# Optimization experiments

Hardware: AMD Instinct MI355X
Metric: run time of the kernel (lower is better)

Reference implementation:

```python
import jax, jax.numpy as jnp
import numpy as np

B, N, D, NS, H, ITERS = 16, 2048, 128, 8, 128, 3
EPS = 1e-8


def _ln(x, g, b):
    m = jnp.mean(x, -1, keepdims=True)
    v = jnp.mean((x - m) ** 2, -1, keepdims=True)
    return (x - m) * jax.lax.rsqrt(v + 1e-5) * g + b


def _gru(x, h, Wih, Whh, bih, bhh):
    # PyTorch GRUCell math
    gi = x @ Wih.T + bih
    gh = h @ Whh.T + bhh
    ir, iz, inn = jnp.split(gi, 3, -1)
    hr, hz, hn = jnp.split(gh, 3, -1)
    r = jax.nn.sigmoid(ir + hr)
    z = jax.nn.sigmoid(iz + hz)
    n = jnp.tanh(inn + r * hn)
    return (1.0 - z) * n + z * h


def setup_inputs() -> dict:
    key = jax.random.key(0)
    ks = jax.random.split(key, 16)

    def lin(k, out_d, in_d):
        lim = 1.0 / np.sqrt(in_d)
        return jax.random.uniform(k, (out_d, in_d), jnp.float32, -lim, lim)

    return {
        "inputs": jax.random.normal(ks[0], (B, N, D), jnp.float32),
        "init_noise": jax.random.normal(ks[1], (B, NS, 2 * D), jnp.float32),
        "slots_mu": jax.random.normal(ks[2], (1, 1, 2 * D), jnp.float32),
        "slots_logsigma": jax.random.normal(ks[3], (1, 1, 2 * D), jnp.float32) * 0.08,  # ~xavier scale
        "Wq": lin(ks[4], D, D),
        "Wk": lin(ks[5], D, D),
        "gru_Wih": lin(ks[6], 3 * D, D),
        "gru_Whh": lin(ks[7], 3 * D, D),
        "gru_bih": jnp.zeros((3 * D,), jnp.float32),
        "gru_bhh": jnp.zeros((3 * D,), jnp.float32),
        "mlp_mu_W1": lin(ks[8], H, D),
        "mlp_mu_b1": jnp.zeros((H,), jnp.float32),
        "mlp_mu_W2": lin(ks[9], D, H),
        "mlp_mu_b2": jnp.zeros((D,), jnp.float32),
        "ln_in_g": jnp.ones((D,), jnp.float32),
        "ln_in_b": jnp.zeros((D,), jnp.float32),
        "ln_slots_g": jnp.ones((2 * D,), jnp.float32),
        "ln_slots_b": jnp.zeros((2 * D,), jnp.float32),
        "ln_mu_g": jnp.ones((D,), jnp.float32),
        "ln_mu_b": jnp.zeros((D,), jnp.float32),
        "mlp_out_W1": lin(ks[10], 2 * H, 2 * D),
        "mlp_out_b1": jnp.zeros((2 * H,), jnp.float32),
        "mlp_out_W2": lin(ks[11], D, 2 * H),
        "mlp_out_b2": jnp.zeros((D,), jnp.float32),
    }


def _forward(inputs, init_noise, slots_mu, slots_logsigma, Wq, Wk,
             gru_Wih, gru_Whh, gru_bih, gru_bhh,
             mlp_mu_W1, mlp_mu_b1, mlp_mu_W2, mlp_mu_b2,
             ln_in_g, ln_in_b, ln_slots_g, ln_slots_b, ln_mu_g, ln_mu_b,
             mlp_out_W1, mlp_out_b1, mlp_out_W2, mlp_out_b2):
    x = _ln(inputs, ln_in_g, ln_in_b)                      # (B,N,D)
    k = x @ Wk.T
    v = k                                                  # original uses to_k for both k and v
    slots = slots_mu + jnp.exp(slots_logsigma) * init_noise  # (B,NS,2D)
    pi_cl = jnp.full((B, NS, 1), 1.0 / NS, inputs.dtype)

    def step(slots, pi_cl):
        s = _ln(slots, ln_slots_g, ln_slots_b)
        mu_s, ls_s = jnp.split(s, 2, -1)                   # (B,NS,D) each
        q_mu = mu_s @ Wq.T
        q_ls = ls_s @ Wq.T
        inv_var = jnp.exp(-2.0 * q_ls)                     # 1 / exp(q_logsigma)^2
        diff = k[:, None, :, :] - q_mu[:, :, None, :]      # (B,NS,N,D)
        dots = jnp.einsum('bind,bid->bin', diff * diff, inv_var)
        dots_exp = (jnp.exp(-dots) + EPS) * pi_cl          # (B,NS,N)
        gammas = dots_exp / dots_exp.sum(1, keepdims=True)
        attn = gammas / gammas.sum(-1, keepdims=True)
        upd = jnp.einsum('bjd,bij->bid', v, attn)          # (B,NS,D)
        upd = _gru(upd.reshape(-1, D), mu_s.reshape(-1, D),
                   gru_Wih, gru_Whh, gru_bih, gru_bhh).reshape(B, NS, D)
        h = _ln(upd, ln_mu_g, ln_mu_b)
        upd = upd + (jax.nn.relu(h @ mlp_mu_W1.T + mlp_mu_b1) @ mlp_mu_W2.T + mlp_mu_b2)
        diff2 = v[:, None, :, :] - upd[:, :, None, :]      # (B,NS,N,D)
        upd_ls = 0.5 * jnp.log(jnp.einsum('bind,bin->bid', diff2 * diff2 + EPS, attn))
        slots_new = jnp.concatenate([upd, upd_ls], -1)
        pi_new = gammas.sum(-1, keepdims=True)
        pi_new = pi_new / pi_new.shape[2]                  # shape[2]==1: faithful no-op from original
        return slots_new, pi_new

    for _ in range(ITERS):
        slots, pi_cl = step(slots, pi_cl)
    slots, pi_cl = step(jax.lax.stop_gradient(slots), pi_cl)
    h = jax.nn.relu(slots @ mlp_out_W1.T + mlp_out_b1)
    return h @ mlp_out_W2.T + mlp_out_b2                   # (B,NS,D)


def reference(inputs, init_noise, slots_mu, slots_logsigma, Wq, Wk,
              gru_Wih, gru_Whh, gru_bih, gru_bhh,
              mlp_mu_W1, mlp_mu_b1, mlp_mu_W2, mlp_mu_b2,
              ln_in_g, ln_in_b, ln_slots_g, ln_slots_b, ln_mu_g, ln_mu_b,
              mlp_out_W1, mlp_out_b1, mlp_out_W2, mlp_out_b2):
    return _forward(inputs, init_noise, slots_mu, slots_logsigma, Wq, Wk,
                    gru_Wih, gru_Whh, gru_bih, gru_bhh,
                    mlp_mu_W1, mlp_mu_b1, mlp_mu_W2, mlp_mu_b2,
                    ln_in_g, ln_in_b, ln_slots_g, ln_slots_b, ln_mu_g, ln_mu_b,
                    mlp_out_W1, mlp_out_b1, mlp_out_W2, mlp_out_b2)
```

## Files before the change

### kernel.cpp

```cpp
#include <hip/hip_runtime.h>

#define EPS_ 1e-8f

constexpr int OFF_K     = 0;
constexpr int OFF_WQT   = 4194304;
constexpr int OFF_WKT   = OFF_WQT  + 16384;
constexpr int OFF_WIHT  = OFF_WKT  + 16384;
constexpr int OFF_WHHT  = OFF_WIHT + 49152;
constexpr int OFF_WM1T  = OFF_WHHT + 49152;
constexpr int OFF_WM2T  = OFF_WM1T + 16384;
constexpr int OFF_WO1T  = OFF_WM2T + 16384;
constexpr int OFF_WO2T  = OFF_WO1T + 65536;
constexpr int OFF_SLOTS = OFF_WO2T + 32768;
constexpr int OFF_PI    = OFF_SLOTS+ 32768;
constexpr int OFF_MUS   = OFF_PI   + 128;
constexpr int OFF_WA    = OFF_MUS  + 16384;
constexpr int OFF_WB    = OFF_WA   + 16384;
constexpr int OFF_UN    = OFF_WB   + 16384;
constexpr int OFF_S2    = OFF_UN   + 524288;
constexpr int OFF_DEN   = OFF_S2   + 524288;
constexpr int OFF_CZ    = OFF_DEN  + 4096;

__global__ __launch_bounds__(256) void init_kernel(
    const float* __restrict__ Wq,  const float* __restrict__ Wk,
    const float* __restrict__ Wih, const float* __restrict__ Whh,
    const float* __restrict__ Wm1, const float* __restrict__ Wm2,
    const float* __restrict__ Wo1, const float* __restrict__ Wo2,
    const float* __restrict__ smu, const float* __restrict__ sls,
    const float* __restrict__ noise, float* __restrict__ ws) {
  int idx = blockIdx.x * 256 + threadIdx.x;
  if (idx < 16384) { int j = idx >> 7, d = idx & 127; ws[OFF_WQT + d*128 + j] = Wq[idx]; return; }
  idx -= 16384;
  if (idx < 16384) { int j = idx >> 7, d = idx & 127; ws[OFF_WKT + d*128 + j] = Wk[idx]; return; }
  idx -= 16384;
  if (idx < 49152) { int j = idx >> 7, d = idx & 127; ws[OFF_WIHT + d*384 + j] = Wih[idx]; return; }
  idx -= 49152;
  if (idx < 49152) { int j = idx >> 7, d = idx & 127; ws[OFF_WHHT + d*384 + j] = Whh[idx]; return; }
  idx -= 49152;
  if (idx < 16384) { int j = idx >> 7, d = idx & 127; ws[OFF_WM1T + d*128 + j] = Wm1[idx]; return; }
  idx -= 16384;
  if (idx < 16384) { int j = idx >> 7, d = idx & 127; ws[OFF_WM2T + d*128 + j] = Wm2[idx]; return; }
  idx -= 16384;
  if (idx < 65536) { int j = idx >> 8, d = idx & 255; ws[OFF_WO1T + d*256 + j] = Wo1[idx]; return; }
  idx -= 65536;
  if (idx < 32768) { int j = idx >> 8, m = idx & 255; ws[OFF_WO2T + m*128 + j] = Wo2[idx]; return; }
  idx -= 32768;
  if (idx < 32768) { int c = idx & 255; ws[OFF_SLOTS + idx] = smu[c] + expf(sls[c]) * noise[idx]; return; }
  idx -= 32768;
  if (idx < 128) { ws[OFF_PI + idx] = 0.125f; }
}

__global__ __launch_bounds__(256) void ks1_kernel(
    const float* __restrict__ xin, const float* __restrict__ g, const float* __restrict__ bb,
    const float* __restrict__ WkT, float* __restrict__ kout,
    const float* __restrict__ slots, const float* __restrict__ gsl, const float* __restrict__ bsl,
    const float* __restrict__ WqT, float* __restrict__ mus,
    float* __restrict__ wA, float* __restrict__ wB, float* __restrict__ cz) {
  __shared__ float xsT[128][72];
  __shared__ float2 red2[64][4];
  __shared__ float mrow[64], srow[64];
  int t = threadIdx.x;
  if (blockIdx.x < 512) {
    long long base = (long long)blockIdx.x * 64 * 128;
    int r = t >> 2, q = t & 3;
    float vals[32];
    {
      const float4* src = (const float4*)(xin + base + r * 128 + q * 32);
      #pragma unroll
      for (int i = 0; i < 8; ++i) *(float4*)&vals[i * 4] = src[i];
    }
    {
      float s = 0.f, ss = 0.f;
      #pragma unroll
      for (int i = 0; i < 32; ++i) { float v = vals[i]; s += v; ss = fmaf(v, v, ss); }
      red2[r][q] = make_float2(s, ss);
    }
    __syncthreads();
    if (t < 64) {
      float s = 0.f, ss = 0.f;
      #pragma unroll
      for (int c = 0; c < 4; ++c) { float2 p = red2[t][c]; s += p.x; ss += p.y; }
      float m = s * (1.0f / 128.0f);
      float var = ss * (1.0f / 128.0f) - m * m;
      mrow[t] = m; srow[t] = rsqrtf(var + 1e-5f);
    }
    __syncthreads();
    {
      float m = mrow[r], is = srow[r];
      #pragma unroll 8
      for (int u = 0; u < 32; ++u) {
        int d = q * 32 + u;
        xsT[d][r] = (vals[u] - m) * is * g[d] + bb[d];
      }
    }
    __syncthreads();
    int j4 = t & 31, rg = t >> 5;
    int r0 = rg * 8;
    float a0[8], a1[8], a2[8], a3[8];
    #pragma unroll
    for (int i = 0; i < 8; ++i) { a0[i] = 0.f; a1[i] = 0.f; a2[i] = 0.f; a3[i] = 0.f; }
    #pragma unroll 2
    for (int d = 0; d < 128; ++d) {
      float4 wv = *(const float4*)(WkT + d * 128 + j4 * 4);
      float4 x0 = *(const float4*)&xsT[d][r0];
      float4 x1 = *(const float4*)&xsT[d][r0 + 4];
      a0[0] = fmaf(x0.x, wv.x, a0[0]); a1[0] = fmaf(x0.x, wv.y, a1[0]);
      a2[0] = fmaf(x0.x, wv.z, a2[0]); a3[0] = fmaf(x0.x, wv.w, a3[0]);
      a0[1] = fmaf(x0.y, wv.x, a0[1]); a1[1] = fmaf(x0.y, wv.y, a1[1]);
      a2[1] = fmaf(x0.y, wv.z, a2[1]); a3[1] = fmaf(x0.y, wv.w, a3[1]);
      a0[2] = fmaf(x0.z, wv.x, a0[2]); a1[2] = fmaf(x0.z, wv.y, a1[2]);
      a2[2] = fmaf(x0.z, wv.z, a2[2]); a3[2] = fmaf(x0.z, wv.w, a3[2]);
      a0[3] = fmaf(x0.w, wv.x, a0[3]); a1[3] = fmaf(x0.w, wv.y, a1[3]);
      a2[3] = fmaf(x0.w, wv.z, a2[3]); a3[3] = fmaf(x0.w, wv.w, a3[3]);
      a0[4] = fmaf(x1.x, wv.x, a0[4]); a1[4] = fmaf(x1.x, wv.y, a1[4]);
      a2[4] = fmaf(x1.x, wv.z, a2[4]); a3[4] = fmaf(x1.x, wv.w, a3[4]);
      a0[5] = fmaf(x1.y, wv.x, a0[5]); a1[5] = fmaf(x1.y, wv.y, a1[5]);
      a2[5] = fmaf(x1.y, wv.z, a2[5]); a3[5] = fmaf(x1.y, wv.w, a3[5]);
      a0[6] = fmaf(x1.z, wv.x, a0[6]); a1[6] = fmaf(x1.z, wv.y, a1[6]);
      a2[6] = fmaf(x1.z, wv.z, a2[6]); a3[6] = fmaf(x1.z, wv.w, a3[6]);
      a0[7] = fmaf(x1.w, wv.x, a0[7]); a1[7] = fmaf(x1.w, wv.y, a1[7]);
      a2[7] = fmaf(x1.w, wv.z, a2[7]); a3[7] = fmaf(x1.w, wv.w, a3[7]);
    }
    #pragma unroll
    for (int i = 0; i < 8; ++i) {
      float* o = kout + base + (long long)(r0 + i) * 128 + j4 * 4;
      *(float4*)o = make_float4(a0[i], a1[i], a2[i], a3[i]);
    }
  } else {
    int bi = blockIdx.x - 512;
    float* f = &xsT[0][0];
    float* sl    = f;
    float* qs_l  = f + 256;
    float* ivs_l = f + 384;
    float2* wr   = (float2*)(f + 512);
    float* wrC   = f + 520;
    float v = slots[bi * 256 + t];
    float s = v, ss = v * v;
    #pragma unroll
    for (int o = 32; o > 0; o >>= 1) { s += __shfl_down(s, o); ss += __shfl_down(ss, o); }
    if ((t & 63) == 0) wr[t >> 6] = make_float2(s, ss);
    __syncthreads();
    float fs  = wr[0].x + wr[1].x + wr[2].x + wr[3].x;
    float fss = wr[0].y + wr[1].y + wr[2].y + wr[3].y;
    float m   = fs * (1.0f/256.0f);
    float var = fss * (1.0f/256.0f) - m * m;
    float isr = rsqrtf(var + 1e-5f);
    float sn  = (v - m) * isr * gsl[t] + bsl[t];
    sl[t] = sn;
    __syncthreads();
    if (t < 128) {
      float acc = 0.f;
      #pragma unroll 4
      for (int d = 0; d < 128; ++d) acc = fmaf(sl[d], WqT[d * 128 + t], acc);
      qs_l[t] = acc;
      mus[bi * 128 + t] = sn;
    } else {
      int jj = t - 128;
      float acc = 0.f;
      #pragma unroll 4
      for (int d = 0; d < 128; ++d) acc = fmaf(sl[128 + d], WqT[d * 128 + jj], acc);
      ivs_l[jj] = expf(-2.0f * acc);
    }
    __syncthreads();
    float cp = 0.f;
    if (t < 128) {
      float iv = ivs_l[t], q = qs_l[t];
      wA[bi * 128 + t] = iv;
      wB[bi * 128 + t] = -2.0f * q * iv;
      cp = q * q * iv;
    }
    #pragma unroll
    for (int o = 32; o > 0; o >>= 1) cp += __shfl_down(cp, o);
    if ((t & 63) == 0) wrC[t >> 6] = cp;
    __syncthreads();
    if (t == 0) cz[bi] = wrC[0] + wrC[1];
  }
}

__global__ __launch_bounds__(1024) void s2_kernel(
    const float* __restrict__ kmat, const float* __restrict__ wA,
    const float* __restrict__ wB,  const float* __restrict__ cz,
    const float* __restrict__ pi,
    float* __restrict__ wun, float* __restrict__ ws2, float* __restrict__ wden) {
  __shared__ float pdots[16][64][8];
  __shared__ float es[64][9];
  __shared__ float recip[64];
  __shared__ float gT[8][72];
  __shared__ float pd[8][8];
  __shared__ float pisl[8], czl[8];
  int t = threadIdx.x;
  int chunk = blockIdx.x, b = blockIdx.y;
  if (t < 8) { pisl[t] = pi[b * 8 + t]; czl[t] = cz[b * 8 + t]; }
  if (t < 512) {
    int w = t & 15, nt = t >> 4;
    int n0 = nt * 2;
    const float4* kr4 = (const float4*)(kmat + (long long)(b * 2048 + chunk * 64) * 128);
    const float4* wa4 = (const float4*)(wA + b * 1024);
    const float4* wb4 = (const float4*)(wB + b * 1024);
    float acc0[8] = {0,0,0,0,0,0,0,0};
    float acc1[8] = {0,0,0,0,0,0,0,0};
    #pragma unroll
    for (int i = 0; i < 2; ++i) {
      int gg = i * 16 + w;
      float4 k0 = kr4[n0 * 32 + gg];
      float4 k1 = kr4[(n0 + 1) * 32 + gg];
      float x0 = k0.x * k0.x, y0 = k0.y * k0.y, z0 = k0.z * k0.z, w0 = k0.w * k0.w;
      float x1 = k1.x * k1.x, y1 = k1.y * k1.y, z1 = k1.z * k1.z, w1 = k1.w * k1.w;
      #pragma unroll
      for (int s = 0; s < 8; ++s) {
        float4 a4 = wa4[s * 32 + gg];
        float4 b4 = wb4[s * 32 + gg];
        float c0 = acc0[s], c1 = acc1[s];
        c0 = fmaf(x0, a4.x, c0); c0 = fmaf(k0.x, b4.x, c0);
        c0 = fmaf(y0, a4.y, c0); c0 = fmaf(k0.y, b4.y, c0);
        c0 = fmaf(z0, a4.z, c0); c0 = fmaf(k0.z, b4.z, c0);
        c0 = fmaf(w0, a4.w, c0); c0 = fmaf(k0.w, b4.w, c0);
        c1 = fmaf(x1, a4.x, c1); c1 = fmaf(k1.x, b4.x, c1);
        c1 = fmaf(y1, a4.y, c1); c1 = fmaf(k1.y, b4.y, c1);
        c1 = fmaf(z1, a4.z, c1); c1 = fmaf(k1.z, b4.z, c1);
        c1 = fmaf(w1, a4.w, c1); c1 = fmaf(k1.w, b4.w, c1);
        acc0[s] = c0; acc1[s] = c1;
      }
    }
    *(float4*)&pdots[w][n0][0]     = make_float4(acc0[0], acc0[1], acc0[2], acc0[3]);
    *(float4*)&pdots[w][n0][4]     = make_float4(acc0[4], acc0[5], acc0[6], acc0[7]);
    *(float4*)&pdots[w][n0 + 1][0] = make_float4(acc1[0], acc1[1], acc1[2], acc1[3]);
    *(float4*)&pdots[w][n0 + 1][4] = make_float4(acc1[4], acc1[5], acc1[6], acc1[7]);
  }
  __syncthreads();
  float e = 0.f;
  if (t < 512) {
    int n2 = t >> 3, s = t & 7;
    float dots = czl[s];
    #pragma unroll
    for (int w = 0; w < 16; ++w) dots += pdots[w][n2][s];
    e = (expf(-dots) + EPS_) * pisl[s];
    es[n2][s] = e;
  }
  __syncthreads();
  if (t < 64) {
    float ssum = 0.f;
    #pragma unroll
    for (int s = 0; s < 8; ++s) ssum += es[t][s];
    recip[t] = 1.0f / ssum;
  }
  __syncthreads();
  if (t < 512) {
    int n2 = t >> 3, s = t & 7;
    float gam = e * recip[n2];
    gT[s][n2] = gam;
    float p = gam;
    p += __shfl_down(p, 8); p += __shfl_down(p, 16); p += __shfl_down(p, 32);
    if ((t & 63) < 8) pd[t >> 6][t & 7] = p;
  }
  __syncthreads();
  if (t < 8) {
    float sden = 0.f;
    #pragma unroll
    for (int w = 0; w < 8; ++w) sden += pd[w][t];
    wden[(b * 32 + chunk) * 8 + t] = sden;
  }
  {
    int d = t & 127, sh = t >> 7;
    const float* kcol = kmat + (long long)(b * 2048 + chunk * 64) * 128 + d;
    float u0 = 0.f, q0 = 0.f, u1 = 0.f, q1 = 0.f;
    #pragma unroll 2
    for (int n3 = 0; n3 < 64; n3 += 4) {
      float4 ga = *(const float4*)&gT[sh][n3];
      float k0 = kcol[(n3 + 0) * 128];
      float k1 = kcol[(n3 + 1) * 128];
      float k2 = kcol[(n3 + 2) * 128];
      float k3 = kcol[(n3 + 3) * 128];
      u0 = fmaf(ga.x, k0, u0); q0 = fmaf(ga.x, k0 * k0, q0);
      u1 = fmaf(ga.y, k1, u1); q1 = fmaf(ga.y, k1 * k1, q1);
      u0 = fmaf(ga.z, k2, u0); q0 = fmaf(ga.z, k2 * k2, q0);
      u1 = fmaf(ga.w, k3, u1); q1 = fmaf(ga.w, k3 * k3, q1);
    }
    int pb = ((b * 32 + chunk) * 8 + sh) * 128 + d;
    wun[pb] = u0 + u1;
    ws2[pb] = q0 + q1;
  }
}

__global__ __launch_bounds__(512) void s3_kernel(
    const float* __restrict__ wun, const float* __restrict__ ws2, const float* __restrict__ wden,
    const float* __restrict__ WihT, const float* __restrict__ WhhT,
    const float* __restrict__ bih,  const float* __restrict__ bhh,
    const float* __restrict__ Wm1T, const float* __restrict__ bm1,
    const float* __restrict__ Wm2T, const float* __restrict__ bm2,
    const float* __restrict__ gmu,  const float* __restrict__ bmu,
    float* __restrict__ slots, float* __restrict__ pi,
    int do_s1,
    const float* __restrict__ gs, const float* __restrict__ bs,
    const float* __restrict__ WqT,
    float* __restrict__ mus, float* __restrict__ wAo, float* __restrict__ wBo,
    float* __restrict__ czo,
    const float* __restrict__ Wo1T, const float* __restrict__ bo1,
    const float* __restrict__ Wo2T, const float* __restrict__ bo2,
    float* __restrict__ out) {
  int t = threadIdx.x, bi = blockIdx.x;
  int d = t & 127, q = t >> 7;
  int b = bi >> 3, i = bi & 7;
  __shared__ float redU[4][128], redS[4][128];
  __shared__ float dred[32];
  __shared__ float xs[128], hs[128];
  __shared__ float gacc[4][6][128];
  __shared__ float ga[6][128];
  __shared__ float grus[128], hl[128], m1s[128];
  __shared__ float macc[4][128];
  __shared__ float2 wr2[2];
  __shared__ float uarr[256];
  float unp = 0.f, s2p = 0.f;
  #pragma unroll
  for (int c = q * 8; c < q * 8 + 8; ++c) {
    int po = ((b * 32 + c) * 8 + i) * 128 + d;
    unp += wun[po]; s2p += ws2[po];
  }
  redU[q][d] = unp; redS[q][d] = s2p;
  if (t < 32) dred[t] = wden[(b * 32 + t) * 8 + i];
  if (q == 1) hs[d] = mus[bi * 128 + d];
  __syncthreads();
  float den = 0.f;
  #pragma unroll
  for (int c = 0; c < 32; ++c) den += dred[c];
  float un  = redU[0][d] + redU[1][d] + redU[2][d] + redU[3][d];
  float s2v = redS[0][d] + redS[1][d] + redS[2][d] + redS[3][d];
  if (q == 0) xs[d] = un / den;
  __syncthreads();
  {
    float a0 = 0, a1 = 0, a2 = 0, a3 = 0, a4 = 0, a5 = 0;
    #pragma unroll 4
    for (int dd = q * 32; dd < q * 32 + 32; ++dd) {
      float xv = xs[dd], hv = hs[dd];
      const float* wi = &WihT[dd * 384 + d];
      const float* wh = &WhhT[dd * 384 + d];
      a0 = fmaf(xv, wi[0],   a0);
      a1 = fmaf(xv, wi[128], a1);
      a2 = fmaf(xv, wi[256], a2);
      a3 = fmaf(hv, wh[0],   a3);
      a4 = fmaf(hv, wh[128], a4);
      a5 = fmaf(hv, wh[256], a5);
    }
    gacc[q][0][d] = a0; gacc[q][1][d] = a1; gacc[q][2][d] = a2;
    gacc[q][3][d] = a3; gacc[q][4][d] = a4; gacc[q][5][d] = a5;
  }
  __syncthreads();
  for (int f = t; f < 768; f += 512) {
    int j = f >> 7, dd = f & 127;
    ga[j][dd] = gacc[0][j][dd] + gacc[1][j][dd] + gacc[2][j][dd] + gacc[3][j][dd];
  }
  __syncthreads();
  float gru = 0.f;
  if (q == 0) {
    float ir = ga[0][d] + bih[d], iz = ga[1][d] + bih[128 + d], inn = ga[2][d] + bih[256 + d];
    float hr = ga[3][d] + bhh[d], hz = ga[4][d] + bhh[128 + d], hn  = ga[5][d] + bhh[256 + d];
    float r  = 1.0f / (1.0f + expf(-(ir + hr)));
    float z  = 1.0f / (1.0f + expf(-(iz + hz)));
    float nn = tanhf(inn + r * hn);
    gru = (1.0f - z) * nn + z * hs[d];
    grus[d] = gru;
    float s = gru, ssq = gru * gru;
    #pragma unroll
    for (int o = 32; o > 0; o >>= 1) { s += __shfl_down(s, o); ssq += __shfl_down(ssq, o); }
    if ((d & 63) == 0) wr2[d >> 6] = make_float2(s, ssq);
  }
  __syncthreads();
  if (q == 0) {
    float fs = wr2[0].x + wr2[1].x, fss = wr2[0].y + wr2[1].y;
    float mean = fs * (1.0f/128.0f);
    float var  = fss * (1.0f/128.0f) - mean * mean;
    hl[d] = (gru - mean) * rsqrtf(var + 1e-5f) * gmu[d] + bmu[d];
  }
  __syncthreads();
  {
    float m1p = 0.f;
    #pragma unroll 4
    for (int dd = q * 32; dd < q * 32 + 32; ++dd)
      m1p = fmaf(hl[dd], Wm1T[dd * 128 + d], m1p);
    macc[q][d] = m1p;
  }
  __syncthreads();
  if (q == 0) m1s[d] = fmaxf(macc[0][d] + macc[1][d] + macc[2][d] + macc[3][d] + bm1[d], 0.f);
  __syncthreads();
  {
    float m2p = 0.f;
    #pragma unroll 4
    for (int dd = q * 32; dd < q * 32 + 32; ++dd)
      m2p = fmaf(m1s[dd], Wm2T[dd * 128 + d], m2p);
    macc[q][d] = m2p;
  }
  __syncthreads();
  if (q == 0) {
    float u = grus[d] + macc[0][d] + macc[1][d] + macc[2][d] + macc[3][d] + bm2[d];
    float val = (s2v - 2.0f * u * un + u * u * den) / den;
    float ls = 0.5f * logf(fmaxf(val, 0.0f) + EPS_);
    slots[bi * 256 + d]       = u;
    slots[bi * 256 + 128 + d] = ls;
    uarr[d] = u; uarr[128 + d] = ls;
    if (d == 0) pi[bi] = den;
  }
  __syncthreads();
  if (do_s1) {
    __shared__ float2 wr4[4];
    __shared__ float sln[256];
    __shared__ float qacc[2][2][128];
    __shared__ float qs_l[128], ivs_l[128];
    __shared__ float wrC[8];
    if (t < 256) {
      float v2 = uarr[t];
      float s = v2, ssq = v2 * v2;
      #pragma unroll
      for (int o = 32; o > 0; o >>= 1) { s += __shfl_down(s, o); ssq += __shfl_down(ssq, o); }
      if ((t & 63) == 0) wr4[t >> 6] = make_float2(s, ssq);
    }
    __syncthreads();
    if (t < 256) {
      float fs  = wr4[0].x + wr4[1].x + wr4[2].x + wr4[3].x;
      float fss = wr4[0].y + wr4[1].y + wr4[2].y + wr4[3].y;
      float m   = fs * (1.0f/256.0f);
      float var = fss * (1.0f/256.0f) - m * m;
      sln[t] = (uarr[t] - m) * rsqrtf(var + 1e-5f) * gs[t] + bs[t];
    }
    __syncthreads();
    {
      int h2 = t >> 8, qq = (t >> 7) & 1, d2 = t & 127;
      const float* src = sln + h2 * 128;
      float acc = 0.f;
      #pragma unroll 4
      for (int dd = qq * 64; dd < qq * 64 + 64; ++dd)
        acc = fmaf(src[dd], WqT[dd * 128 + d2], acc);
      qacc[h2][qq][d2] = acc;
    }
    __syncthreads();
    if (t < 128) {
      qs_l[t] = qacc[0][0][t] + qacc[0][1][t];
      mus[bi * 128 + t] = sln[t];
    } else if (t < 256) {
      int dd2 = t - 128;
      ivs_l[dd2] = expf(-2.0f * (qacc[1][0][dd2] + qacc[1][1][dd2]));
    }
    __syncthreads();
    float cp = 0.f;
    if (t < 128) {
      float iv = ivs_l[t], qv = qs_l[t];
      wAo[bi * 128 + t] = iv;
      wBo[bi * 128 + t] = -2.0f * qv * iv;
      cp = qv * qv * iv;
    }
    #pragma unroll
    for (int o = 32; o > 0; o >>= 1) cp += __shfl_down(cp, o);
    if ((t & 63) == 0) wrC[t >> 6] = cp;
    __syncthreads();
    if (t == 0) czo[bi] = wrC[0] + wrC[1];
  } else {
    __shared__ float oacc[2][256];
    __shared__ float hh[256];
    {
      int o = t & 255, qq = t >> 8;
      float acc = 0.f;
      #pragma unroll 4
      for (int dd = qq * 128; dd < qq * 128 + 128; ++dd)
        acc = fmaf(uarr[dd], Wo1T[dd * 256 + o], acc);
      oacc[qq][o] = acc;
    }
    __syncthreads();
    if (t < 256) hh[t] = fmaxf(oacc[0][t] + oacc[1][t] + bo1[t], 0.f);
    __syncthreads();
    {
      int o2 = t & 127, q4 = t >> 7;
      float acc2 = 0.f;
      #pragma unroll 4
      for (int dd = q4 * 64; dd < q4 * 64 + 64; ++dd)
        acc2 = fmaf(hh[dd], Wo2T[dd * 128 + o2], acc2);
      macc[q4][o2] = acc2;
    }
    __syncthreads();
    if (t < 128) out[bi * 128 + t] = macc[0][t] + macc[1][t] + macc[2][t] + macc[3][t] + bo2[t];
  }
}

extern "C" void kernel_launch(void* const* d_in, const int* in_sizes, int n_in,
                              void* d_out, int out_size, void* d_ws, size_t ws_size,
                              hipStream_t stream) {
  const float* inputs = (const float*)d_in[0];
  const float* noise  = (const float*)d_in[1];
  const float* smu    = (const float*)d_in[2];
  const float* sls    = (const float*)d_in[3];
  const float* Wq     = (const float*)d_in[4];
  const float* Wk     = (const float*)d_in[5];
  const float* Wih    = (const float*)d_in[6];
  const float* Whh    = (const float*)d_in[7];
  const float* bih    = (const float*)d_in[8];
  const float* bhh    = (const float*)d_in[9];
  const float* Wm1    = (const float*)d_in[10];
  const float* bm1    = (const float*)d_in[11];
  const float* Wm2    = (const float*)d_in[12];
  const float* bm2    = (const float*)d_in[13];
  const float* gin    = (const float*)d_in[14];
  const float* bin    = (const float*)d_in[15];
  const float* gsl    = (const float*)d_in[16];
  const float* bsl    = (const float*)d_in[17];
  const float* gmu    = (const float*)d_in[18];
  const float* bmu    = (const float*)d_in[19];
  const float* Wo1    = (const float*)d_in[20];
  const float* bo1    = (const float*)d_in[21];
  const float* Wo2    = (const float*)d_in[22];
  const float* bo2    = (const float*)d_in[23];

  float* ws    = (float*)d_ws;
  float* kbuf  = ws + OFF_K;
  float* WqT   = ws + OFF_WQT;
  float* WkT   = ws + OFF_WKT;
  float* WihT  = ws + OFF_WIHT;
  float* WhhT  = ws + OFF_WHHT;
  float* Wm1T  = ws + OFF_WM1T;
  float* Wm2T  = ws + OFF_WM2T;
  float* Wo1T  = ws + OFF_WO1T;
  float* Wo2T  = ws + OFF_WO2T;
  float* slots = ws + OFF_SLOTS;
  float* pibuf = ws + OFF_PI;
  float* mus   = ws + OFF_MUS;
  float* wA    = ws + OFF_WA;
  float* wB    = ws + OFF_WB;
  float* wun   = ws + OFF_UN;
  float* ws2   = ws + OFF_S2;
  float* wden  = ws + OFF_DEN;
  float* czb   = ws + OFF_CZ;

  hipLaunchKernelGGL(init_kernel, dim3(1153), dim3(256), 0, stream,
                     Wq, Wk, Wih, Whh, Wm1, Wm2, Wo1, Wo2, smu, sls, noise, ws);
  hipLaunchKernelGGL(ks1_kernel, dim3(640), dim3(256), 0, stream,
                     inputs, gin, bin, WkT, kbuf,
                     slots, gsl, bsl, WqT, mus, wA, wB, czb);
  for (int s = 0; s < 4; ++s) {
    hipLaunchKernelGGL(s2_kernel, dim3(32, 16), dim3(1024), 0, stream,
                       kbuf, wA, wB, czb, pibuf, wun, ws2, wden);
    hipLaunchKernelGGL(s3_kernel, dim3(128), dim3(512), 0, stream,
                       wun, ws2, wden, WihT, WhhT, bih, bhh,
                       Wm1T, bm1, Wm2T, bm2, gmu, bmu, slots, pibuf,
                       (s < 3) ? 1 : 0, gsl, bsl, WqT, mus, wA, wB, czb,
                       Wo1T, bo1, Wo2T, bo2, (float*)d_out);
  }
}
```

Measured before the change: 174.9 us.

## Fuse s2 and s3 into one step kernel using a last-block atomic counter

Merges the per-chunk responsibility/statistics kernel and the per-slot GRU/MLP update kernel into a single launch per iteration. The last block to finish for each batch, detected with an atomic counter and threadfence, performs the slot update for all 8 slots. This removes four kernel launches and their inter-kernel gaps. The update stage now runs on only 16 blocks with serial 128-long reductions instead of 128 blocks, so that tail work may lengthen. The u/s2 accumulation is also rewritten to read k with coalesced float4 loads and reduce partials in shared memory.

```diff
diff --git a/kernel.cpp b/kernel.cpp
--- a/kernel.cpp
+++ b/kernel.cpp
@@ -20,6 +20,15 @@
 constexpr int OFF_S2    = OFF_UN   + 524288;
 constexpr int OFF_DEN   = OFF_S2   + 524288;
 constexpr int OFF_CZ    = OFF_DEN  + 4096;
+constexpr int OFF_CNT   = OFF_CZ   + 128;
+
+struct Args {
+  const float *xin, *noise, *smu, *sls, *Wq, *Wk, *Wih, *Whh, *bih, *bhh,
+              *Wm1, *bm1, *Wm2, *bm2, *gin, *bin, *gsl, *bsl, *gmu, *bmu,
+              *Wo1, *bo1, *Wo2, *bo2;
+  float* ws;
+  float* out;
+};
 
 __global__ __launch_bounds__(256) void init_kernel(
     const float* __restrict__ Wq,  const float* __restrict__ Wk,
@@ -47,7 +56,9 @@
   idx -= 32768;
   if (idx < 32768) { int c = idx & 255; ws[OFF_SLOTS + idx] = smu[c] + expf(sls[c]) * noise[idx]; return; }
   idx -= 32768;
-  if (idx < 128) { ws[OFF_PI + idx] = 0.125f; }
+  if (idx < 128) { ws[OFF_PI + idx] = 0.125f; return; }
+  idx -= 128;
+  if (idx < 64) { ((int*)(ws + OFF_CNT))[idx] = 0; }
 }
 
 __global__ __launch_bounds__(256) void ks1_kernel(
@@ -177,20 +188,44 @@
   }
 }
 
-__global__ __launch_bounds__(1024) void s2_kernel(
-    const float* __restrict__ kmat, const float* __restrict__ wA,
-    const float* __restrict__ wB,  const float* __restrict__ cz,
-    const float* __restrict__ pi,
-    float* __restrict__ wun, float* __restrict__ ws2, float* __restrict__ wden) {
-  __shared__ float pdots[16][64][8];
+struct ScrS3 {
+  float xs[8][128];
+  float hs[8][128];
+  float gh[2][8][128];
+  float m1s[8][128];
+  float uarr[8][256];
+  float2 wr2[8][2];
+  float wrC[8][2];
+};
+union UScr {
+  struct { float pdots[16][64][8]; } p1;
+  struct { float pP[2][4][8][128]; } p2;
+  ScrS3 s3;
+};
+
+__global__ __launch_bounds__(1024) void step_kernel(Args a, int step) {
+  float* ws = a.ws;
+  const float* kmat = ws + OFF_K;
+  float* wA  = ws + OFF_WA;  float* wB  = ws + OFF_WB;
+  float* czp = ws + OFF_CZ;  float* pip = ws + OFF_PI;
+  float* wun = ws + OFF_UN;  float* ws2 = ws + OFF_S2;
+  float* wden= ws + OFF_DEN; float* mus = ws + OFF_MUS;
+  const float* WihT = ws + OFF_WIHT; const float* WhhT = ws + OFF_WHHT;
+  const float* Wm1T = ws + OFF_WM1T; const float* Wm2T = ws + OFF_WM2T;
+  const float* WqT  = ws + OFF_WQT;
+  const float* Wo1T = ws + OFF_WO1T; const float* Wo2T = ws + OFF_WO2T;
+  float* slots = ws + OFF_SLOTS;
+
+  __shared__ UScr u;
   __shared__ float es[64][9];
   __shared__ float recip[64];
   __shared__ float gT[8][72];
   __shared__ float pd[8][8];
   __shared__ float pisl[8], czl[8];
+  __shared__ int sflag;
   int t = threadIdx.x;
   int chunk = blockIdx.x, b = blockIdx.y;
-  if (t < 8) { pisl[t] = pi[b * 8 + t]; czl[t] = cz[b * 8 + t]; }
+  if (t < 8) { pisl[t] = pip[b * 8 + t]; czl[t] = czp[b * 8 + t]; }
   if (t < 512) {
     int w = t & 15, nt = t >> 4;
     int n0 = nt * 2;
@@ -222,10 +257,10 @@
         acc0[s] = c0; acc1[s] = c1;
       }
     }
-    *(float4*)&pdots[w][n0][0]     = make_float4(acc0[0], acc0[1], acc0[2], acc0[3]);
-    *(float4*)&pdots[w][n0][4]     = make_float4(acc0[4], acc0[5], acc0[6], acc0[7]);
-    *(float4*)&pdots[w][n0 + 1][0] = make_float4(acc1[0], acc1[1], acc1[2], acc1[3]);
-    *(float4*)&pdots[w][n0 + 1][4] = make_float4(acc1[4], acc1[5], acc1[6], acc1[7]);
+    *(float4*)&u.p1.pdots[w][n0][0]     = make_float4(acc0[0], acc0[1], acc0[2], acc0[3]);
+    *(float4*)&u.p1.pdots[w][n0][4]     = make_float4(acc0[4], acc0[5], acc0[6], acc0[7]);
+    *(float4*)&u.p1.pdots[w][n0 + 1][0] = make_float4(acc1[0], acc1[1], acc1[2], acc1[3]);
+    *(float4*)&u.p1.pdots[w][n0 + 1][4] = make_float4(acc1[4], acc1[5], acc1[6], acc1[7]);
   }
   __syncthreads();
   float e = 0.f;
@@ -233,7 +268,7 @@
     int n2 = t >> 3, s = t & 7;
     float dots = czl[s];
     #pragma unroll
-    for (int w = 0; w < 16; ++w) dots += pdots[w][n2][s];
+    for (int w = 0; w < 16; ++w) dots += u.p1.pdots[w][n2][s];
     e = (expf(-dots) + EPS_) * pisl[s];
     es[n2][s] = e;
   }
@@ -261,284 +296,198 @@
     wden[(b * 32 + chunk) * 8 + t] = sden;
   }
   {
-    int d = t & 127, sh = t >> 7;
-    const float* kcol = kmat + (long long)(b * 2048 + chunk * 64) * 128 + d;
-    float u0 = 0.f, q0 = 0.f, u1 = 0.f, q1 = 0.f;
+    int g = t & 31, sl = (t >> 5) & 7, nh = t >> 8;
+    const float4* kr4 = (const float4*)(kmat + (long long)(b * 2048 + chunk * 64) * 128);
+    float4 ua = {0, 0, 0, 0}, qa = {0, 0, 0, 0};
     #pragma unroll 2
-    for (int n3 = 0; n3 < 64; n3 += 4) {
-      float4 ga = *(const float4*)&gT[sh][n3];
-      float k0 = kcol[(n3 + 0) * 128];
-      float k1 = kcol[(n3 + 1) * 128];
-      float k2 = kcol[(n3 + 2) * 128];
-      float k3 = kcol[(n3 + 3) * 128];
-      u0 = fmaf(ga.x, k0, u0); q0 = fmaf(ga.x, k0 * k0, q0);
-      u1 = fmaf(ga.y, k1, u1); q1 = fmaf(ga.y, k1 * k1, q1);
-      u0 = fmaf(ga.z, k2, u0); q0 = fmaf(ga.z, k2 * k2, q0);
-      u1 = fmaf(ga.w, k3, u1); q1 = fmaf(ga.w, k3 * k3, q1);
-    }
-    int pb = ((b * 32 + chunk) * 8 + sh) * 128 + d;
-    wun[pb] = u0 + u1;
-    ws2[pb] = q0 + q1;
-  }
-}
-
-__global__ __launch_bounds__(512) void s3_kernel(
-    const float* __restrict__ wun, const float* __restrict__ ws2, const float* __restrict__ wden,
-    const float* __restrict__ WihT, const float* __restrict__ WhhT,
-    const float* __restrict__ bih,  const float* __restrict__ bhh,
-    const float* __restrict__ Wm1T, const float* __restrict__ bm1,
-    const float* __restrict__ Wm2T, const float* __restrict__ bm2,
-    const float* __restrict__ gmu,  const float* __restrict__ bmu,
-    float* __restrict__ slots, float* __restrict__ pi,
-    int do_s1,
-    const float* __restrict__ gs, const float* __restrict__ bs,
-    const float* __restrict__ WqT,
-    float* __restrict__ mus, float* __restrict__ wAo, float* __restrict__ wBo,
-    float* __restrict__ czo,
-    const float* __restrict__ Wo1T, const float* __restrict__ bo1,
-    const float* __restrict__ Wo2T, const float* __restrict__ bo2,
-    float* __restrict__ out) {
-  int t = threadIdx.x, bi = blockIdx.x;
-  int d = t & 127, q = t >> 7;
-  int b = bi >> 3, i = bi & 7;
-  __shared__ float redU[4][128], redS[4][128];
-  __shared__ float dred[32];
-  __shared__ float xs[128], hs[128];
-  __shared__ float gacc[4][6][128];
-  __shared__ float ga[6][128];
-  __shared__ float grus[128], hl[128], m1s[128];
-  __shared__ float macc[4][128];
-  __shared__ float2 wr2[2];
-  __shared__ float uarr[256];
-  float unp = 0.f, s2p = 0.f;
-  #pragma unroll
-  for (int c = q * 8; c < q * 8 + 8; ++c) {
-    int po = ((b * 32 + c) * 8 + i) * 128 + d;
-    unp += wun[po]; s2p += ws2[po];
-  }
-  redU[q][d] = unp; redS[q][d] = s2p;
-  if (t < 32) dred[t] = wden[(b * 32 + t) * 8 + i];
-  if (q == 1) hs[d] = mus[bi * 128 + d];
-  __syncthreads();
-  float den = 0.f;
-  #pragma unroll
-  for (int c = 0; c < 32; ++c) den += dred[c];
-  float un  = redU[0][d] + redU[1][d] + redU[2][d] + redU[3][d];
-  float s2v = redS[0][d] + redS[1][d] + redS[2][d] + redS[3][d];
-  if (q == 0) xs[d] = un / den;
-  __syncthreads();
-  {
-    float a0 = 0, a1 = 0, a2 = 0, a3 = 0, a4 = 0, a5 = 0;
+    for (int n = nh * 16; n < nh * 16 + 16; ++n) {
+      float4 kv = kr4[n * 32 + g];
+      float gam = gT[sl][n];
+      ua.x = fmaf(gam, kv.x, ua.x); qa.x = fmaf(gam, kv.x * kv.x, qa.x);
+      ua.y = fmaf(gam, kv.y, ua.y); qa.y = fmaf(gam, kv.y * kv.y, qa.y);
+      ua.z = fmaf(gam, kv.z, ua.z); qa.z = fmaf(gam, kv.z * kv.z, qa.z);
+      ua.w = fmaf(gam, kv.w, ua.w); qa.w = fmaf(gam, kv.w * kv.w, qa.w);
+    }
+    *(float4*)&u.p2.pP[0][nh][sl][g * 4] = ua;
+    *(float4*)&u.p2.pP[1][nh][sl][g * 4] = qa;
+  }
+  __syncthreads();
+  {
+    int uq = t >> 9, rem = t & 511;
+    int sl = rem >> 6, d0 = (rem & 63) * 2;
+    float* dst = (uq == 0 ? wun : ws2);
+    long long pbase = (long long)((b * 32 + chunk) * 8 + sl) * 128;
+    #pragma unroll
+    for (int eo = 0; eo < 2; ++eo) {
+      int d = d0 + eo;
+      dst[pbase + d] = u.p2.pP[uq][0][sl][d] + u.p2.pP[uq][1][sl][d] +
+                       u.p2.pP[uq][2][sl][d] + u.p2.pP[uq][3][sl][d];
+    }
+  }
+  __syncthreads();
+  if (t == 0) {
+    __threadfence();
+    sflag = atomicAdd((int*)(ws + OFF_CNT) + step * 16 + b, 1);
+  }
+  __syncthreads();
+  if (sflag != 31) return;
+  __threadfence();
+  ScrS3* p = &u.s3;
+  int i = t >> 7, d = t & 127, bi = b * 8 + i;
+  float un = 0.f, s2v = 0.f, den = 0.f;
+  for (int c = 0; c < 32; ++c) {
+    long long po = (long long)((b * 32 + c) * 8 + i) * 128 + d;
+    un += wun[po]; s2v += ws2[po];
+  }
+  for (int c = 0; c < 32; ++c) den += wden[(b * 32 + c) * 8 + i];
+  p->xs[i][d] = un / den;
+  p->hs[i][d] = mus[bi * 128 + d];
+  __syncthreads();
+  float a0 = 0, a1 = 0, a2 = 0, a3 = 0, a4 = 0, a5 = 0;
+  #pragma unroll 2
+  for (int dd = 0; dd < 128; ++dd) {
+    float xv = p->xs[i][dd], hv = p->hs[i][dd];
+    const float* wi = &WihT[dd * 384 + d];
+    const float* wh = &WhhT[dd * 384 + d];
+    a0 = fmaf(xv, wi[0],   a0);
+    a1 = fmaf(xv, wi[128], a1);
+    a2 = fmaf(xv, wi[256], a2);
+    a3 = fmaf(hv, wh[0],   a3);
+    a4 = fmaf(hv, wh[128], a4);
+    a5 = fmaf(hv, wh[256], a5);
+  }
+  float ir = a0 + a.bih[d], iz = a1 + a.bih[128 + d], inn = a2 + a.bih[256 + d];
+  float hr = a3 + a.bhh[d], hz = a4 + a.bhh[128 + d], hn  = a5 + a.bhh[256 + d];
+  float rg = 1.0f / (1.0f + expf(-(ir + hr)));
+  float zg = 1.0f / (1.0f + expf(-(iz + hz)));
+  float nn = tanhf(inn + rg * hn);
+  float gru = (1.0f - zg) * nn + zg * p->hs[i][d];
+  p->gh[0][i][d] = gru;
+  {
+    float s = gru, ssq = gru * gru;
+    #pragma unroll
+    for (int o = 32; o > 0; o >>= 1) { s += __shfl_down(s, o); ssq += __shfl_down(ssq, o); }
+    if ((d & 63) == 0) p->wr2[i][d >> 6] = make_float2(s, ssq);
+  }
+  __syncthreads();
+  {
+    float fs = p->wr2[i][0].x + p->wr2[i][1].x;
+    float fss = p->wr2[i][0].y + p->wr2[i][1].y;
+    float mean = fs * (1.0f / 128.0f);
+    float var  = fss * (1.0f / 128.0f) - mean * mean;
+    p->gh[1][i][d] = (gru - mean) * rsqrtf(var + 1e-5f) * a.gmu[d] + a.bmu[d];
+  }
+  __syncthreads();
+  {
+    float m1 = 0.f;
     #pragma unroll 4
-    for (int dd = q * 32; dd < q * 32 + 32; ++dd) {
-      float xv = xs[dd], hv = hs[dd];
-      const float* wi = &WihT[dd * 384 + d];
-      const float* wh = &WhhT[dd * 384 + d];
-      a0 = fmaf(xv, wi[0],   a0);
-      a1 = fmaf(xv, wi[128], a1);
-      a2 = fmaf(xv, wi[256], a2);
-      a3 = fmaf(hv, wh[0],   a3);
-      a4 = fmaf(hv, wh[128], a4);
-      a5 = fmaf(hv, wh[256], a5);
-    }
-    gacc[q][0][d] = a0; gacc[q][1][d] = a1; gacc[q][2][d] = a2;
-    gacc[q][3][d] = a3; gacc[q][4][d] = a4; gacc[q][5][d] = a5;
-  }
-  __syncthreads();
-  for (int f = t; f < 768; f += 512) {
-    int j = f >> 7, dd = f & 127;
-    ga[j][dd] = gacc[0][j][dd] + gacc[1][j][dd] + gacc[2][j][dd] + gacc[3][j][dd];
-  }
-  __syncthreads();
-  float gru = 0.f;
-  if (q == 0) {
-    float ir = ga[0][d] + bih[d], iz = ga[1][d] + bih[128 + d], inn = ga[2][d] + bih[256 + d];
-    float hr = ga[3][d] + bhh[d], hz = ga[4][d] + bhh[128 + d], hn  = ga[5][d] + bhh[256 + d];
-    float r  = 1.0f / (1.0f + expf(-(ir + hr)));
-    float z  = 1.0f / (1.0f + expf(-(iz + hz)));
-    float nn = tanhf(inn + r * hn);
-    gru = (1.0f - z) * nn + z * hs[d];
-    grus[d] = gru;
-    float s = gru, ssq = gru * gru;
-    #pragma unroll
-    for (int o = 32; o > 0; o >>= 1) { s += __shfl_down(s, o); ssq += __shfl_down(ssq, o); }
-    if ((d & 63) == 0) wr2[d >> 6] = make_float2(s, ssq);
-  }
-  __syncthreads();
-  if (q == 0) {
-    float fs = wr2[0].x + wr2[1].x, fss = wr2[0].y + wr2[1].y;
-    float mean = fs * (1.0f/128.0f);
-    float var  = fss * (1.0f/128.0f) - mean * mean;
-    hl[d] = (gru - mean) * rsqrtf(var + 1e-5f) * gmu[d] + bmu[d];
-  }
-  __syncthreads();
-  {
-    float m1p = 0.f;
+    for (int dd = 0; dd < 128; ++dd)
+      m1 = fmaf(p->gh[1][i][dd], Wm1T[dd * 128 + d], m1);
+    p->m1s[i][d] = fmaxf(m1 + a.bm1[d], 0.f);
+  }
+  __syncthreads();
+  float uu, lsv;
+  {
+    float m2 = 0.f;
     #pragma unroll 4
-    for (int dd = q * 32; dd < q * 32 + 32; ++dd)
-      m1p = fmaf(hl[dd], Wm1T[dd * 128 + d], m1p);
-    macc[q][d] = m1p;
-  }
-  __syncthreads();
-  if (q == 0) m1s[d] = fmaxf(macc[0][d] + macc[1][d] + macc[2][d] + macc[3][d] + bm1[d], 0.f);
-  __syncthreads();
-  {
-    float m2p = 0.f;
-    #pragma unroll 4
-    for (int dd = q * 32; dd < q * 32 + 32; ++dd)
-      m2p = fmaf(m1s[dd], Wm2T[dd * 128 + d], m2p);
-    macc[q][d] = m2p;
-  }
-  __syncthreads();
-  if (q == 0) {
-    float u = grus[d] + macc[0][d] + macc[1][d] + macc[2][d] + macc[3][d] + bm2[d];
-    float val = (s2v - 2.0f * u * un + u * u * den) / den;
-    float ls = 0.5f * logf(fmaxf(val, 0.0f) + EPS_);
-    slots[bi * 256 + d]       = u;
-    slots[bi * 256 + 128 + d] = ls;
-    uarr[d] = u; uarr[128 + d] = ls;
-    if (d == 0) pi[bi] = den;
-  }
-  __syncthreads();
-  if (do_s1) {
-    __shared__ float2 wr4[4];
-    __shared__ float sln[256];
-    __shared__ float qacc[2][2][128];
-    __shared__ float qs_l[128], ivs_l[128];
-    __shared__ float wrC[8];
-    if (t < 256) {
-      float v2 = uarr[t];
-      float s = v2, ssq = v2 * v2;
+    for (int dd = 0; dd < 128; ++dd)
+      m2 = fmaf(p->m1s[i][dd], Wm2T[dd * 128 + d], m2);
+    uu = gru + m2 + a.bm2[d];
+    float val = (s2v - 2.0f * uu * un + uu * uu * den) / den;
+    lsv = 0.5f * logf(fmaxf(val, 0.0f) + EPS_);
+  }
+  __syncthreads();
+  slots[bi * 256 + d]       = uu;
+  slots[bi * 256 + 128 + d] = lsv;
+  p->uarr[i][d] = uu; p->uarr[i][128 + d] = lsv;
+  if (d == 0) pip[bi] = den;
+  __syncthreads();
+  float* ov = &p->gh[0][0][0];
+  if (step < 3) {
+    float v0 = p->uarr[i][d], v1 = p->uarr[i][128 + d];
+    {
+      float s = v0 + v1, ssq = v0 * v0 + v1 * v1;
       #pragma unroll
       for (int o = 32; o > 0; o >>= 1) { s += __shfl_down(s, o); ssq += __shfl_down(ssq, o); }
-      if ((t & 63) == 0) wr4[t >> 6] = make_float2(s, ssq);
-    }
-    __syncthreads();
-    if (t < 256) {
-      float fs  = wr4[0].x + wr4[1].x + wr4[2].x + wr4[3].x;
-      float fss = wr4[0].y + wr4[1].y + wr4[2].y + wr4[3].y;
-      float m   = fs * (1.0f/256.0f);
-      float var = fss * (1.0f/256.0f) - m * m;
-      sln[t] = (uarr[t] - m) * rsqrtf(var + 1e-5f) * gs[t] + bs[t];
-    }
-    __syncthreads();
+      if ((d & 63) == 0) p->wr2[i][d >> 6] = make_float2(s, ssq);
+    }
+    __syncthreads();
+    float* sln = ov + i * 256;
     {
-      int h2 = t >> 8, qq = (t >> 7) & 1, d2 = t & 127;
-      const float* src = sln + h2 * 128;
-      float acc = 0.f;
-      #pragma unroll 4
-      for (int dd = qq * 64; dd < qq * 64 + 64; ++dd)
-        acc = fmaf(src[dd], WqT[dd * 128 + d2], acc);
-      qacc[h2][qq][d2] = acc;
-    }
-    __syncthreads();
-    if (t < 128) {
-      qs_l[t] = qacc[0][0][t] + qacc[0][1][t];
-      mus[bi * 128 + t] = sln[t];
-    } else if (t < 256) {
-      int dd2 = t - 128;
-      ivs_l[dd2] = expf(-2.0f * (qacc[1][0][dd2] + qacc[1][1][dd2]));
-    }
-    __syncthreads();
-    float cp = 0.f;
-    if (t < 128) {
-      float iv = ivs_l[t], qv = qs_l[t];
-      wAo[bi * 128 + t] = iv;
-      wBo[bi * 128 + t] = -2.0f * qv * iv;
-      cp = qv * qv * iv;
-    }
+      float fs = p->wr2[i][0].x + p->wr2[i][1].x;
+      float fss = p->wr2[i][0].y + p->wr2[i][1].y;
+      float m = fs * (1.0f / 256.0f);
+      float var = fss * (1.0f / 256.0f) - m * m;
+      float isr = rsqrtf(var + 1e-5f);
+      sln[d]       = (v0 - m) * isr * a.gsl[d] + a.bsl[d];
+      sln[128 + d] = (v1 - m) * isr * a.gsl[128 + d] + a.bsl[128 + d];
+    }
+    __syncthreads();
+    float qacc = 0.f, iacc = 0.f;
+    #pragma unroll 4
+    for (int dd = 0; dd < 128; ++dd) {
+      float wv = WqT[dd * 128 + d];
+      qacc = fmaf(sln[dd],       wv, qacc);
+      iacc = fmaf(sln[128 + dd], wv, iacc);
+    }
+    float iv = expf(-2.0f * iacc);
+    wA[bi * 128 + d] = iv;
+    wB[bi * 128 + d] = -2.0f * qacc * iv;
+    mus[bi * 128 + d] = sln[d];
+    float cp = qacc * qacc * iv;
     #pragma unroll
     for (int o = 32; o > 0; o >>= 1) cp += __shfl_down(cp, o);
-    if ((t & 63) == 0) wrC[t >> 6] = cp;
-    __syncthreads();
-    if (t == 0) czo[bi] = wrC[0] + wrC[1];
+    if ((d & 63) == 0) p->wrC[i][d >> 6] = cp;
+    __syncthreads();
+    if (d == 0) czp[bi] = p->wrC[i][0] + p->wrC[i][1];
   } else {
-    __shared__ float oacc[2][256];
-    __shared__ float hh[256];
-    {
-      int o = t & 255, qq = t >> 8;
-      float acc = 0.f;
-      #pragma unroll 4
-      for (int dd = qq * 128; dd < qq * 128 + 128; ++dd)
-        acc = fmaf(uarr[dd], Wo1T[dd * 256 + o], acc);
-      oacc[qq][o] = acc;
-    }
-    __syncthreads();
-    if (t < 256) hh[t] = fmaxf(oacc[0][t] + oacc[1][t] + bo1[t], 0.f);
-    __syncthreads();
-    {
-      int o2 = t & 127, q4 = t >> 7;
-      float acc2 = 0.f;
-      #pragma unroll 4
-      for (int dd = q4 * 64; dd < q4 * 64 + 64; ++dd)
-        acc2 = fmaf(hh[dd], Wo2T[dd * 128 + o2], acc2);
-      macc[q4][o2] = acc2;
-    }
-    __syncthreads();
-    if (t < 128) out[bi * 128 + t] = macc[0][t] + macc[1][t] + macc[2][t] + macc[3][t] + bo2[t];
+    float* hh = ov + i * 256;
+    float acc0 = 0.f, acc1 = 0.f;
+    #pragma unroll 4
+    for (int dd = 0; dd < 256; ++dd) {
+      float uv = p->uarr[i][dd];
+      acc0 = fmaf(uv, Wo1T[dd * 256 + d],       acc0);
+      acc1 = fmaf(uv, Wo1T[dd * 256 + 128 + d], acc1);
+    }
+    hh[d]       = fmaxf(acc0 + a.bo1[d], 0.f);
+    hh[128 + d] = fmaxf(acc1 + a.bo1[128 + d], 0.f);
+    __syncthreads();
+    float o = 0.f;
+    #pragma unroll 4
+    for (int dd = 0; dd < 256; ++dd)
+      o = fmaf(hh[dd], Wo2T[dd * 128 + d], o);
+    a.out[bi * 128 + d] = o + a.bo2[d];
   }
 }
 
 extern "C" void kernel_launch(void* const* d_in, const int* in_sizes, int n_in,
                               void* d_out, int out_size, void* d_ws, size_t ws_size,
                               hipStream_t stream) {
-  const float* inputs = (const float*)d_in[0];
-  const float* noise  = (const float*)d_in[1];
-  const float* smu    = (const float*)d_in[2];
-  const float* sls    = (const float*)d_in[3];
-  const float* Wq     = (const float*)d_in[4];
-  const float* Wk     = (const float*)d_in[5];
-  const float* Wih    = (const float*)d_in[6];
-  const float* Whh    = (const float*)d_in[7];
-  const float* bih    = (const float*)d_in[8];
-  const float* bhh    = (const float*)d_in[9];
-  const float* Wm1    = (const float*)d_in[10];
-  const float* bm1    = (const float*)d_in[11];
-  const float* Wm2    = (const float*)d_in[12];
-  const float* bm2    = (const float*)d_in[13];
-  const float* gin    = (const float*)d_in[14];
-  const float* bin    = (const float*)d_in[15];
-  const float* gsl    = (const float*)d_in[16];
-  const float* bsl    = (const float*)d_in[17];
-  const float* gmu    = (const float*)d_in[18];
-  const float* bmu    = (const float*)d_in[19];
-  const float* Wo1    = (const float*)d_in[20];
-  const float* bo1    = (const float*)d_in[21];
-  const float* Wo2    = (const float*)d_in[22];
-  const float* bo2    = (const float*)d_in[23];
-
-  float* ws    = (float*)d_ws;
-  float* kbuf  = ws + OFF_K;
-  float* WqT   = ws + OFF_WQT;
-  float* WkT   = ws + OFF_WKT;
-  float* WihT  = ws + OFF_WIHT;
-  float* WhhT  = ws + OFF_WHHT;
-  float* Wm1T  = ws + OFF_WM1T;
-  float* Wm2T  = ws + OFF_WM2T;
-  float* Wo1T  = ws + OFF_WO1T;
-  float* Wo2T  = ws + OFF_WO2T;
-  float* slots = ws + OFF_SLOTS;
-  float* pibuf = ws + OFF_PI;
-  float* mus   = ws + OFF_MUS;
-  float* wA    = ws + OFF_WA;
-  float* wB    = ws + OFF_WB;
-  float* wun   = ws + OFF_UN;
-  float* ws2   = ws + OFF_S2;
-  float* wden  = ws + OFF_DEN;
-  float* czb   = ws + OFF_CZ;
-
+  Args a;
+  a.xin  = (const float*)d_in[0];  a.noise = (const float*)d_in[1];
+  a.smu  = (const float*)d_in[2];  a.sls   = (const float*)d_in[3];
+  a.Wq   = (const float*)d_in[4];  a.Wk    = (const float*)d_in[5];
+  a.Wih  = (const float*)d_in[6];  a.Whh   = (const float*)d_in[7];
+  a.bih  = (const float*)d_in[8];  a.bhh   = (const float*)d_in[9];
+  a.Wm1  = (const float*)d_in[10]; a.bm1   = (const float*)d_in[11];
+  a.Wm2  = (const float*)d_in[12]; a.bm2   = (const float*)d_in[13];
+  a.gin  = (const float*)d_in[14]; a.bin   = (const float*)d_in[15];
+  a.gsl  = (const float*)d_in[16]; a.bsl   = (const float*)d_in[17];
+  a.gmu  = (const float*)d_in[18]; a.bmu   = (const float*)d_in[19];
+  a.Wo1  = (const float*)d_in[20]; a.bo1   = (const float*)d_in[21];
+  a.Wo2  = (const float*)d_in[22]; a.bo2   = (const float*)d_in[23];
+  a.ws   = (float*)d_ws;
+  a.out  = (float*)d_out;
+
+  float* ws = (float*)d_ws;
   hipLaunchKernelGGL(init_kernel, dim3(1153), dim3(256), 0, stream,
-                     Wq, Wk, Wih, Whh, Wm1, Wm2, Wo1, Wo2, smu, sls, noise, ws);
+                     a.Wq, a.Wk, a.Wih, a.Whh, a.Wm1, a.Wm2, a.Wo1, a.Wo2,
+                     a.smu, a.sls, a.noise, ws);
   hipLaunchKernelGGL(ks1_kernel, dim3(640), dim3(256), 0, stream,
-                     inputs, gin, bin, WkT, kbuf,
-                     slots, gsl, bsl, WqT, mus, wA, wB, czb);
+                     a.xin, a.gin, a.bin, ws + OFF_WKT, ws + OFF_K,
+                     ws + OFF_SLOTS, a.gsl, a.bsl, ws + OFF_WQT,
+                     ws + OFF_MUS, ws + OFF_WA, ws + OFF_WB, ws + OFF_CZ);
   for (int s = 0; s < 4; ++s) {
-    hipLaunchKernelGGL(s2_kernel, dim3(32, 16), dim3(1024), 0, stream,
-                       kbuf, wA, wB, czb, pibuf, wun, ws2, wden);
-    hipLaunchKernelGGL(s3_kernel, dim3(128), dim3(512), 0, stream,
-                       wun, ws2, wden, WihT, WhhT, bih, bhh,
-                       Wm1T, bm1, Wm2T, bm2, gmu, bmu, slots, pibuf,
-                       (s < 3) ? 1 : 0, gsl, bsl, WqT, mus, wA, wB, czb,
-                       Wo1T, bo1, Wo2T, bo2, (float*)d_out);
+    hipLaunchKernelGGL(step_kernel, dim3(32, 16), dim3(1024), 0, stream, a, s);
   }
 }
```

After: 483.7 us. 2.77x slower.
